# Performance work log

Measured on AMD Instinct MI355X. Metric: run time of the kernel, lower is better.

Reference implementation:

```python
import jax, jax.numpy as jnp
import numpy as np

B, N, D = 4, 2048, 256
EPS = 1e-5


def _clinear(Z, W, b):
    # complex linear: Z (B,2,N,din), W (2,dout,din), b (2,dout)
    Zr, Zi = Z[:, 0], Z[:, 1]
    Wr, Wi = W[0], W[1]
    outr = Zr @ Wr.T - Zi @ Wi.T + b[0]
    outi = Zr @ Wi.T + Zi @ Wr.T + b[1]
    return jnp.stack([outr, outi], axis=1)


def setup_inputs() -> dict:
    key = jax.random.key(0)
    ks = jax.random.split(key, 14)
    sc = 1.0 / np.sqrt(D).astype(np.float32)
    t = jnp.tile(jnp.arange(N + 1, dtype=jnp.float32)[None] * 0.01, (B, 1))
    return {
        'Z_q': jax.random.normal(ks[0], (B, 2, N, D), jnp.float32),
        'Z_k': jax.random.normal(ks[1], (B, 2, N, D), jnp.float32),
        'Z_v': jax.random.normal(ks[2], (B, 2, N, D), jnp.float32),
        't_measure_all': t,
        'W_q': jax.random.normal(ks[3], (2, D, D), jnp.float32) * sc,
        'b_q': jax.random.normal(ks[4], (2, D), jnp.float32) * 0.01,
        'W_k': jax.random.normal(ks[5], (2, D, D), jnp.float32) * sc,
        'b_k': jax.random.normal(ks[6], (2, D), jnp.float32) * 0.01,
        'W_v': jax.random.normal(ks[7], (2, D, D), jnp.float32) * sc,
        'b_v': jax.random.normal(ks[8], (2, D), jnp.float32) * 0.01,
        'W_p': jax.random.normal(ks[9], (2, D, D), jnp.float32) * sc,
        'b_p': jax.random.normal(ks[10], (2, D), jnp.float32) * 0.01,
        'lambda1': jax.random.normal(ks[11], (2, D // 2, 1), jnp.float32),
        'lambda_Omega_sqrt': jax.random.normal(ks[12], (1, D, 1), jnp.float32) * sc,
        'lambda_Gamma_sqrt': jax.random.normal(ks[13], (1, D, 1), jnp.float32) * sc,
        'tau': jnp.asarray(1.0, jnp.float32),
        'delta': jnp.asarray(0.0, jnp.float32),
        'lambda_C': jnp.ones((1, D, 1), jnp.float32),
    }


def reference(Z_q, Z_k, Z_v, t_measure_all, W_q, b_q, W_k, b_k, W_v, b_v,
              W_p, b_p, lambda1, lambda_Omega_sqrt, lambda_Gamma_sqrt,
              tau, delta, lambda_C):
    # lambda_h = 0 * compute_lambda_h(lambda1): conjugate-pair spectrum, zeroed in forward
    lam_r = 0.0 * jnp.concatenate([lambda1[0], lambda1[0]], axis=0)[:, 0]   # (D,)
    lam_i = 0.0 * jnp.concatenate([lambda1[1], -lambda1[1]], axis=0)[:, 0]  # (D,)
    lam_Om = lambda_Omega_sqrt ** 2 + EPS   # process noise (1,D,1)
    lam_Ga = lambda_Gamma_sqrt ** 2 + EPS   # measurement noise (1,D,1)

    Q = _clinear(Z_q, W_q, b_q)  # (B,2,N,D)
    K = _clinear(Z_k, W_k, b_k)
    V = _clinear(Z_v, W_v, b_v)

    t = t_measure_all[0, :-1]  # (N,)
    # exponential state-transition kernels exp(+/- lambda * t): (2,N,D)
    mag_f = jnp.exp(lam_r[None] * t[:, None]); ph_f = lam_i[None] * t[:, None]
    exp_f = jnp.stack([mag_f * jnp.cos(ph_f), mag_f * jnp.sin(ph_f)])
    mag_b = jnp.exp(-lam_r[None] * t[:, None]); ph_b = -lam_i[None] * t[:, None]
    exp_b = jnp.stack([mag_b * jnp.cos(ph_b), mag_b * jnp.sin(ph_b)])
    # one-step transition exp(lambda * dt): (2,D)
    dt = t[1] - t[0]
    mat_exp = jnp.stack([jnp.exp(lam_r * dt) * jnp.cos(lam_i * dt),
                         jnp.exp(lam_r * dt) * jnp.sin(lam_i * dt)])

    # averaged covariance kernel, exact lambda->0 limit: Gamma + Omega*|t_i-t_j|, mean over D
    lamC2 = lambda_C[0, :, 0] ** 2
    ga_bar = jnp.mean(lamC2 * lam_Ga[0, :, 0])
    om_bar = jnp.mean(lamC2 * lam_Om[0, :, 0])
    abs_dt = jnp.abs(t[:, None] - t[None, :])          # (N,N)
    V_avg_ij = ga_bar + om_bar * abs_dt                # (N,N)

    # factorized kernels
    V_v = exp_f[None]                 # (1,2,N,D)
    U_q = exp_b[None] * Q             # (B,2,N,D)
    U_k = exp_b[None] * K
    U_v = exp_b[None] * V

    # precision-weighted squared residual norm R_ij = sum_d |V_k|^2 |U_q_i - U_k_j|^2
    Vk_abs = jnp.sum(exp_f ** 2, axis=0)              # (N,D)
    Uk_abs = jnp.sum(U_k ** 2, axis=1)                # (B,N,D)
    Uq_abs = jnp.sum(U_q ** 2, axis=1)                # (B,N,D)
    T1 = jnp.einsum('id,bjd->bij', Vk_abs, Uk_abs)
    T2 = jnp.sum(Vk_abs[None] * Uq_abs, axis=2)[:, :, None]
    T3 = (jnp.einsum('bid,bjd->bij', Vk_abs[None] * U_q[:, 0], U_k[:, 0]) +
          jnp.einsum('bid,bjd->bij', Vk_abs[None] * U_q[:, 1], U_k[:, 1]))
    R_qk_abs = T1 + T2 - 2.0 * T3                     # (B,N,N)

    scores = -(tau ** 2) * jnp.log(V_avg_ij[None] + R_qk_abs)
    mask = jnp.tril(jnp.ones((N, N), bool))
    scores = jnp.where(mask[None], scores, -jnp.inf)
    A = jax.nn.softmax(scores, axis=2)                # (B,N,N)
    Q_ij = jnp.stack([A, jnp.zeros_like(A)], axis=1)  # (B,2,N,N)

    # est_inner = complex matmul(Q_ij, U_v); Q imag part is zero
    est_inner = jnp.stack([jnp.einsum('bij,bjd->bid', A, U_v[:, 0]),
                           jnp.einsum('bij,bjd->bid', A, U_v[:, 1])], axis=1)
    est_v = V_v * est_inner          # plain elementwise product, as in source
    s = jax.nn.sigmoid(delta)
    est_eigenbasis = (1.0 - s) * V + s * est_v        # (B,2,N,D)

    # complex Hadamard with one-step transition
    pr = mat_exp[0][None, None] * est_eigenbasis[:, 0] - mat_exp[1][None, None] * est_eigenbasis[:, 1]
    pi = mat_exp[0][None, None] * est_eigenbasis[:, 1] + mat_exp[1][None, None] * est_eigenbasis[:, 0]
    pred_p = jnp.stack([pr, pi], axis=1)
    out = _clinear(pred_p, W_p, b_p)                  # (B,2,N,D)

    lambda_h = jnp.stack([lam_r, lam_i])[..., None]
    return est_eigenbasis, out, Q_ij, V_v, U_v, lambda_h
```

## Files before the change

### kernel.cpp

```cpp
#include <hip/hip_runtime.h>
#include <math.h>

#define BN 4
#define NN 2048
#define DD 256
#define EPSF 1e-5f

typedef __attribute__((ext_vector_type(8))) short bf16x8;
typedef __attribute__((ext_vector_type(4))) float f32x4;

constexpr size_t OFF_EST = 0;
constexpr size_t OFF_OUT = (size_t)BN * 2 * NN * DD;
constexpr size_t OFF_QIJ = OFF_OUT + (size_t)BN * 2 * NN * DD;
constexpr size_t OFF_VV  = OFF_QIJ + (size_t)BN * 2 * NN * NN;
constexpr size_t OFF_UV  = OFF_VV + (size_t)2 * NN * DD;
constexpr size_t OFF_LH  = OFF_UV + (size_t)BN * 2 * NN * DD;

constexpr size_t SCR_Q16 = OFF_QIJ + (size_t)NN * NN;
constexpr size_t SCR_K16 = SCR_Q16 + (size_t)BN * NN * DD / 2;
constexpr size_t SCR_VT16= SCR_K16 + (size_t)BN * NN * DD / 2;
constexpr size_t SCR_VRF = OFF_QIJ + (size_t)3 * NN * NN;
constexpr size_t SCR_QN  = SCR_VRF + (size_t)BN * NN * DD;
constexpr size_t SCR_KN  = SCR_QN + (size_t)BN * NN;
constexpr size_t SCR_L   = SCR_KN + (size_t)BN * NN;
constexpr size_t SCR_SC  = SCR_L + (size_t)BN * NN;

__device__ __forceinline__ short f2bf(float x) {
    union { float f; unsigned u; } v; v.f = x;
    unsigned r = v.u + 0x7fff + ((v.u >> 16) & 1);
    return (short)(r >> 16);
}
__device__ __forceinline__ float bf2f(unsigned short h) {
    union { unsigned u; float f; } v; v.u = ((unsigned)h) << 16;
    return v.f;
}

__global__ void k_prep(const float* __restrict__ tau, const float* __restrict__ delta,
                       const float* __restrict__ lamOm, const float* __restrict__ lamGa,
                       const float* __restrict__ lamC, float* __restrict__ dout) {
    __shared__ float red[8];
    const int t = threadIdx.x;
    float c2 = lamC[t] * lamC[t];
    float ga = c2 * (lamGa[t] * lamGa[t] + EPSF);
    float om = c2 * (lamOm[t] * lamOm[t] + EPSF);
    for (int o = 32; o > 0; o >>= 1) {
        ga += __shfl_down(ga, o, 64);
        om += __shfl_down(om, o, 64);
    }
    if ((t & 63) == 0) { red[t >> 6] = ga; red[4 + (t >> 6)] = om; }
    __syncthreads();
    if (t == 0) {
        float gs = red[0] + red[1] + red[2] + red[3];
        float os = red[4] + red[5] + red[6] + red[7];
        float* scal = dout + SCR_SC;
        scal[0] = tau[0] * tau[0];
        scal[1] = 1.f / (1.f + __expf(-delta[0]));
        scal[2] = gs / 256.f;
        scal[3] = os / 256.f;
    }
    float* L = dout + SCR_L;
    for (int i = t; i < BN * NN; i += 256) L[i] = 0.f;
}

__global__ __launch_bounds__(256) void k_qkv(
    const float* __restrict__ Zq, const float* __restrict__ Zk, const float* __restrict__ Zv,
    const float* __restrict__ Wq, const float* __restrict__ bq,
    const float* __restrict__ Wk, const float* __restrict__ bk,
    const float* __restrict__ Wv, const float* __restrict__ bv,
    float* __restrict__ dout)
{
    __shared__ short Al[128 * 40];
    __shared__ short Bl[128 * 40];
    const int z = blockIdx.z;
    const int d0 = blockIdx.x * 128;
    const int b = blockIdx.y >> 4;
    const int n0 = (blockIdx.y & 15) * 128;
    const float* Z; const float* W; const float* bias; int mode;
    if (z == 0)      { Z = Zq; W = Wq; bias = bq; mode = 0; }
    else if (z == 1) { Z = Zk; W = Wk; bias = bk; mode = 0; }
    else if (z == 2) { Z = Zv; W = Wv; bias = bv; mode = 0; }
    else             { Z = Zv; W = Wv; bias = bv; mode = 1; }

    const int t = threadIdx.x, wave = t >> 6, lane = t & 63, quad = lane >> 4, lm = lane & 15;
    const int wm = (wave >> 1) * 64, wn = (wave & 1) * 64;
    const int srow = t >> 1, sch = (t & 1) * 16;

    f32x4 acc[4][4];
#pragma unroll
    for (int i = 0; i < 4; ++i)
#pragma unroll
        for (int j = 0; j < 4; ++j) acc[i][j] = (f32x4){0.f, 0.f, 0.f, 0.f};

    for (int kt = 0; kt < 16; ++kt) {
        const int c = kt >> 3, kk0 = (kt & 7) * 32;
        const float* Za = Z + ((size_t)((b * 2 + c) * NN + n0 + srow)) * DD + kk0 + sch;
        float4 a0 = *(const float4*)(Za + 0);
        float4 a1 = *(const float4*)(Za + 4);
        float4 a2 = *(const float4*)(Za + 8);
        float4 a3 = *(const float4*)(Za + 12);
        int wc; float sgn;
        if (mode == 0) { wc = c; sgn = c ? -1.f : 1.f; }
        else           { wc = 1 - c; sgn = 1.f; }
        const float* Wa = W + ((size_t)wc * DD + d0 + srow) * DD + kk0 + sch;
        float4 w0 = *(const float4*)(Wa + 0);
        float4 w1 = *(const float4*)(Wa + 4);
        float4 w2 = *(const float4*)(Wa + 8);
        float4 w3 = *(const float4*)(Wa + 12);
        __syncthreads();
        bf16x8 pa0, pa1, pw0, pw1;
        pa0[0]=f2bf(a0.x); pa0[1]=f2bf(a0.y); pa0[2]=f2bf(a0.z); pa0[3]=f2bf(a0.w);
        pa0[4]=f2bf(a1.x); pa0[5]=f2bf(a1.y); pa0[6]=f2bf(a1.z); pa0[7]=f2bf(a1.w);
        pa1[0]=f2bf(a2.x); pa1[1]=f2bf(a2.y); pa1[2]=f2bf(a2.z); pa1[3]=f2bf(a2.w);
        pa1[4]=f2bf(a3.x); pa1[5]=f2bf(a3.y); pa1[6]=f2bf(a3.z); pa1[7]=f2bf(a3.w);
        pw0[0]=f2bf(sgn*w0.x); pw0[1]=f2bf(sgn*w0.y); pw0[2]=f2bf(sgn*w0.z); pw0[3]=f2bf(sgn*w0.w);
        pw0[4]=f2bf(sgn*w1.x); pw0[5]=f2bf(sgn*w1.y); pw0[6]=f2bf(sgn*w1.z); pw0[7]=f2bf(sgn*w1.w);
        pw1[0]=f2bf(sgn*w2.x); pw1[1]=f2bf(sgn*w2.y); pw1[2]=f2bf(sgn*w2.z); pw1[3]=f2bf(sgn*w2.w);
        pw1[4]=f2bf(sgn*w3.x); pw1[5]=f2bf(sgn*w3.y); pw1[6]=f2bf(sgn*w3.z); pw1[7]=f2bf(sgn*w3.w);
        *(bf16x8*)&Al[srow * 40 + sch]     = pa0;
        *(bf16x8*)&Al[srow * 40 + sch + 8] = pa1;
        *(bf16x8*)&Bl[srow * 40 + sch]     = pw0;
        *(bf16x8*)&Bl[srow * 40 + sch + 8] = pw1;
        __syncthreads();
        bf16x8 af[4], bff[4];
#pragma unroll
        for (int mi = 0; mi < 4; ++mi) af[mi] = *(const bf16x8*)&Al[(wm + mi * 16 + lm) * 40 + quad * 8];
#pragma unroll
        for (int nj = 0; nj < 4; ++nj) bff[nj] = *(const bf16x8*)&Bl[(wn + nj * 16 + lm) * 40 + quad * 8];
#pragma unroll
        for (int mi = 0; mi < 4; ++mi)
#pragma unroll
            for (int nj = 0; nj < 4; ++nj)
                acc[mi][nj] = __builtin_amdgcn_mfma_f32_16x16x32_bf16(af[mi], bff[nj], acc[mi][nj], 0, 0, 0);
    }

    const float sval = dout[SCR_SC + 1];
    unsigned short* Q16 = (unsigned short*)(dout + SCR_Q16);
    unsigned short* K16 = (unsigned short*)(dout + SCR_K16);
    float* VRF = dout + SCR_VRF;
    const int bofs = mode ? DD : 0;
#pragma unroll
    for (int mi = 0; mi < 4; ++mi)
#pragma unroll
        for (int r = 0; r < 4; ++r) {
            const int m = n0 + wm + mi * 16 + quad * 4 + r;
#pragma unroll
            for (int nj = 0; nj < 4; ++nj) {
                const int d = d0 + wn + nj * 16 + lm;
                float v = acc[mi][nj][r] + bias[bofs + d];
                const size_t ibd = ((size_t)b * NN + m) * DD + d;
                if (z == 0) Q16[ibd] = (unsigned short)f2bf(v);
                else if (z == 1) K16[ibd] = (unsigned short)f2bf(v);
                else if (z == 2) {
                    VRF[ibd] = v;
                    dout[OFF_UV + ((size_t)(b * 2) * NN + m) * DD + d] = v;
                } else {
                    dout[OFF_EST + ((size_t)(b * 2 + 1) * NN + m) * DD + d] = (1.f - sval) * v;
                }
            }
        }
}

__global__ __launch_bounds__(256) void k_outproj(
    const float* __restrict__ Wp, const float* __restrict__ bp, float* __restrict__ dout)
{
    __shared__ short Al[128 * 40];
    __shared__ short Bl[128 * 40];
    const int z = blockIdx.z;
    const int d0 = blockIdx.x * 128;
    const int b = blockIdx.y >> 4;
    const int n0 = (blockIdx.y & 15) * 128;
    const float* Z = dout + OFF_EST;
    const int mode = z;

    const int t = threadIdx.x, wave = t >> 6, lane = t & 63, quad = lane >> 4, lm = lane & 15;
    const int wm = (wave >> 1) * 64, wn = (wave & 1) * 64;
    const int srow = t >> 1, sch = (t & 1) * 16;

    f32x4 acc[4][4];
#pragma unroll
    for (int i = 0; i < 4; ++i)
#pragma unroll
        for (int j = 0; j < 4; ++j) acc[i][j] = (f32x4){0.f, 0.f, 0.f, 0.f};

    for (int kt = 0; kt < 16; ++kt) {
        const int c = kt >> 3, kk0 = (kt & 7) * 32;
        const float* Za = Z + ((size_t)((b * 2 + c) * NN + n0 + srow)) * DD + kk0 + sch;
        float4 a0 = *(const float4*)(Za + 0);
        float4 a1 = *(const float4*)(Za + 4);
        float4 a2 = *(const float4*)(Za + 8);
        float4 a3 = *(const float4*)(Za + 12);
        int wc; float sgn;
        if (mode == 0) { wc = c; sgn = c ? -1.f : 1.f; }
        else           { wc = 1 - c; sgn = 1.f; }
        const float* Wa = Wp + ((size_t)wc * DD + d0 + srow) * DD + kk0 + sch;
        float4 w0 = *(const float4*)(Wa + 0);
        float4 w1 = *(const float4*)(Wa + 4);
        float4 w2 = *(const float4*)(Wa + 8);
        float4 w3 = *(const float4*)(Wa + 12);
        __syncthreads();
        bf16x8 pa0, pa1, pw0, pw1;
        pa0[0]=f2bf(a0.x); pa0[1]=f2bf(a0.y); pa0[2]=f2bf(a0.z); pa0[3]=f2bf(a0.w);
        pa0[4]=f2bf(a1.x); pa0[5]=f2bf(a1.y); pa0[6]=f2bf(a1.z); pa0[7]=f2bf(a1.w);
        pa1[0]=f2bf(a2.x); pa1[1]=f2bf(a2.y); pa1[2]=f2bf(a2.z); pa1[3]=f2bf(a2.w);
        pa1[4]=f2bf(a3.x); pa1[5]=f2bf(a3.y); pa1[6]=f2bf(a3.z); pa1[7]=f2bf(a3.w);
        pw0[0]=f2bf(sgn*w0.x); pw0[1]=f2bf(sgn*w0.y); pw0[2]=f2bf(sgn*w0.z); pw0[3]=f2bf(sgn*w0.w);
        pw0[4]=f2bf(sgn*w1.x); pw0[5]=f2bf(sgn*w1.y); pw0[6]=f2bf(sgn*w1.z); pw0[7]=f2bf(sgn*w1.w);
        pw1[0]=f2bf(sgn*w2.x); pw1[1]=f2bf(sgn*w2.y); pw1[2]=f2bf(sgn*w2.z); pw1[3]=f2bf(sgn*w2.w);
        pw1[4]=f2bf(sgn*w3.x); pw1[5]=f2bf(sgn*w3.y); pw1[6]=f2bf(sgn*w3.z); pw1[7]=f2bf(sgn*w3.w);
        *(bf16x8*)&Al[srow * 40 + sch]     = pa0;
        *(bf16x8*)&Al[srow * 40 + sch + 8] = pa1;
        *(bf16x8*)&Bl[srow * 40 + sch]     = pw0;
        *(bf16x8*)&Bl[srow * 40 + sch + 8] = pw1;
        __syncthreads();
        bf16x8 af[4], bff[4];
#pragma unroll
        for (int mi = 0; mi < 4; ++mi) af[mi] = *(const bf16x8*)&Al[(wm + mi * 16 + lm) * 40 + quad * 8];
#pragma unroll
        for (int nj = 0; nj < 4; ++nj) bff[nj] = *(const bf16x8*)&Bl[(wn + nj * 16 + lm) * 40 + quad * 8];
#pragma unroll
        for (int mi = 0; mi < 4; ++mi)
#pragma unroll
            for (int nj = 0; nj < 4; ++nj)
                acc[mi][nj] = __builtin_amdgcn_mfma_f32_16x16x32_bf16(af[mi], bff[nj], acc[mi][nj], 0, 0, 0);
    }
    const int bofs = mode ? DD : 0;
#pragma unroll
    for (int mi = 0; mi < 4; ++mi)
#pragma unroll
        for (int r = 0; r < 4; ++r) {
            const int m = n0 + wm + mi * 16 + quad * 4 + r;
#pragma unroll
            for (int nj = 0; nj < 4; ++nj) {
                const int d = d0 + wn + nj * 16 + lm;
                dout[OFF_OUT + ((size_t)(b * 2 + z) * NN + m) * DD + d] =
                    acc[mi][nj][r] + bp[bofs + d];
            }
        }
}

__global__ void k_vtrans(float* __restrict__ dout) {
    __shared__ float T[64][65];
    const int b = blockIdx.z;
    const int nb = blockIdx.x * 64, db = blockIdx.y * 64;
    const float* V = dout + SCR_VRF + (size_t)b * NN * DD;
    unsigned short* VT = (unsigned short*)(dout + SCR_VT16) + (size_t)b * DD * NN;
    const int tr = threadIdx.x >> 4, tc = (threadIdx.x & 15) * 4;
#pragma unroll
    for (int p = 0; p < 4; ++p) {
        float4 v = *(const float4*)&V[(size_t)(nb + tr + p * 16) * DD + db + tc];
        T[tr + p * 16][tc + 0] = v.x; T[tr + p * 16][tc + 1] = v.y;
        T[tr + p * 16][tc + 2] = v.z; T[tr + p * 16][tc + 3] = v.w;
    }
    __syncthreads();
#pragma unroll
    for (int p = 0; p < 4; ++p) {
        const int d = tr + p * 16;
        ushort4 o;
        o.x = (unsigned short)f2bf(T[tc + 0][d]);
        o.y = (unsigned short)f2bf(T[tc + 1][d]);
        o.z = (unsigned short)f2bf(T[tc + 2][d]);
        o.w = (unsigned short)f2bf(T[tc + 3][d]);
        *(ushort4*)&VT[(size_t)(db + d) * NN + nb + tc] = o;
    }
}

__global__ void k_norms(float* __restrict__ dout) {
    const int r = blockIdx.x;
    const unsigned short* src = (const unsigned short*)(dout + (blockIdx.y ? SCR_K16 : SCR_Q16));
    float v = bf2f(src[(size_t)r * DD + threadIdx.x]);
    float p = v * v;
    for (int o = 32; o > 0; o >>= 1) p += __shfl_down(p, o, 64);
    __shared__ float red[4];
    if ((threadIdx.x & 63) == 0) red[threadIdx.x >> 6] = p;
    __syncthreads();
    if (threadIdx.x == 0)
        dout[(blockIdx.y ? SCR_KN : SCR_QN) + r] = red[0] + red[1] + red[2] + red[3];
}

__global__ __launch_bounds__(256) void k_scores(const float* __restrict__ tmeas,
                                                float* __restrict__ dout) {
    __shared__ short Al[128 * 40];
    __shared__ short Bl[128 * 40];
    const int b = blockIdx.y, x = blockIdx.x;
    int ti = (int)((sqrtf(8.f * x + 1.f) - 1.f) * 0.5f);
    while ((ti + 1) * (ti + 2) / 2 <= x) ++ti;
    while (ti * (ti + 1) / 2 > x) --ti;
    const int tj = x - ti * (ti + 1) / 2;
    const int i0 = ti * 128, j0 = tj * 128;
    const unsigned short* Q16 = (const unsigned short*)(dout + SCR_Q16) + (size_t)b * NN * DD;
    const unsigned short* K16 = (const unsigned short*)(dout + SCR_K16) + (size_t)b * NN * DD;
    const int t = threadIdx.x, wave = t >> 6, lane = t & 63, quad = lane >> 4, lm = lane & 15;
    const int wm = (wave >> 1) * 64, wn = (wave & 1) * 64;
    const int srow = t >> 1, sch = (t & 1) * 16;

    f32x4 acc[4][4];
#pragma unroll
    for (int i = 0; i < 4; ++i)
#pragma unroll
        for (int j = 0; j < 4; ++j) acc[i][j] = (f32x4){0.f, 0.f, 0.f, 0.f};

    for (int kt = 0; kt < 8; ++kt) {
        const int kk0 = kt * 32;
        const float4 qv0 = *(const float4*)(const void*)(Q16 + (size_t)(i0 + srow) * DD + kk0 + sch);
        const float4 qv1 = *(const float4*)(const void*)(Q16 + (size_t)(i0 + srow) * DD + kk0 + sch + 8);
        const float4 kv0 = *(const float4*)(const void*)(K16 + (size_t)(j0 + srow) * DD + kk0 + sch);
        const float4 kv1 = *(const float4*)(const void*)(K16 + (size_t)(j0 + srow) * DD + kk0 + sch + 8);
        __syncthreads();
        *(float4*)(void*)&Al[srow * 40 + sch]     = qv0;
        *(float4*)(void*)&Al[srow * 40 + sch + 8] = qv1;
        *(float4*)(void*)&Bl[srow * 40 + sch]     = kv0;
        *(float4*)(void*)&Bl[srow * 40 + sch + 8] = kv1;
        __syncthreads();
        bf16x8 af[4], bff[4];
#pragma unroll
        for (int mi = 0; mi < 4; ++mi) af[mi] = *(const bf16x8*)&Al[(wm + mi * 16 + lm) * 40 + quad * 8];
#pragma unroll
        for (int nj = 0; nj < 4; ++nj) bff[nj] = *(const bf16x8*)&Bl[(wn + nj * 16 + lm) * 40 + quad * 8];
#pragma unroll
        for (int mi = 0; mi < 4; ++mi)
#pragma unroll
            for (int nj = 0; nj < 4; ++nj)
                acc[mi][nj] = __builtin_amdgcn_mfma_f32_16x16x32_bf16(af[mi], bff[nj], acc[mi][nj], 0, 0, 0);
    }

    const float tau2 = dout[SCR_SC + 0], ga = dout[SCR_SC + 2], om = dout[SCR_SC + 3];
    float* Qij = dout + OFF_QIJ + (size_t)b * 2 * NN * NN;
    const float* QN_ = dout + SCR_QN + b * NN;
    const float* KN_ = dout + SCR_KN + b * NN;
    float kn[4], tjv[4]; int jj[4];
#pragma unroll
    for (int nj = 0; nj < 4; ++nj) {
        jj[nj] = j0 + wn + nj * 16 + lm;
        kn[nj] = KN_[jj[nj]];
        tjv[nj] = tmeas[jj[nj]];
    }
#pragma unroll
    for (int mi = 0; mi < 4; ++mi)
#pragma unroll
        for (int r = 0; r < 4; ++r) {
            const int i = i0 + wm + mi * 16 + quad * 4 + r;
            const float qni = QN_[i], tqi = tmeas[i];
            float rs = 0.f;
#pragma unroll
            for (int nj = 0; nj < 4; ++nj) {
                float xx = ga + om * fabsf(tqi - tjv[nj]) + qni + kn[nj] - 2.f * acc[mi][nj][r];
                xx = fmaxf(xx, 1e-30f);
                float w = (tau2 == 1.f) ? (1.f / xx) : __expf(-tau2 * __logf(xx));
                if (jj[nj] > i) w = 0.f;
                Qij[(size_t)i * NN + jj[nj]] = w;
                rs += w;
            }
            rs += __shfl_down(rs, 8, 16); rs += __shfl_down(rs, 4, 16);
            rs += __shfl_down(rs, 2, 16); rs += __shfl_down(rs, 1, 16);
            if (lm == 0) atomicAdd(&dout[SCR_L + b * NN + i], rs);
        }
}

__global__ __launch_bounds__(256) void k_estinner(float* __restrict__ dout) {
    __shared__ short Al[128 * 40];
    __shared__ short Bl[128 * 40];
    const int b = blockIdx.z;
    const int d0 = blockIdx.x * 128;
    int y = blockIdx.y, TI = 0;
    for (;;) { const int nc = (TI + 2) >> 1; if (y < nc) break; y -= nc; ++TI; }
    const int i0 = TI * 128;
    const int kbeg = y * 256;
    const int kend = min(kbeg + 256, (TI + 1) * 128);
    const int nst = (kend - kbeg) >> 5;
    const float* Qij = dout + OFF_QIJ + (size_t)b * 2 * NN * NN;
    const unsigned short* VT = (const unsigned short*)(dout + SCR_VT16) + (size_t)b * DD * NN;

    const int t = threadIdx.x, wave = t >> 6, lane = t & 63, quad = lane >> 4, lm = lane & 15;
    const int wm = (wave >> 1) * 64, wn = (wave & 1) * 64;
    const int srow = t >> 1, sch = (t & 1) * 16;

    f32x4 acc[4][4];
#pragma unroll
    for (int i = 0; i < 4; ++i)
#pragma unroll
        for (int j = 0; j < 4; ++j) acc[i][j] = (f32x4){0.f, 0.f, 0.f, 0.f};

    for (int kt = 0; kt < nst; ++kt) {
        const int kk0 = kbeg + kt * 32;
        const float* Aa = Qij + (size_t)(i0 + srow) * NN + kk0 + sch;
        float4 a0 = *(const float4*)(Aa + 0);
        float4 a1 = *(const float4*)(Aa + 4);
        float4 a2 = *(const float4*)(Aa + 8);
        float4 a3 = *(const float4*)(Aa + 12);
        const float4 bv0 = *(const float4*)(const void*)(VT + (size_t)(d0 + srow) * NN + kk0 + sch);
        const float4 bv1 = *(const float4*)(const void*)(VT + (size_t)(d0 + srow) * NN + kk0 + sch + 8);
        __syncthreads();
        bf16x8 pa0, pa1;
        pa0[0]=f2bf(a0.x); pa0[1]=f2bf(a0.y); pa0[2]=f2bf(a0.z); pa0[3]=f2bf(a0.w);
        pa0[4]=f2bf(a1.x); pa0[5]=f2bf(a1.y); pa0[6]=f2bf(a1.z); pa0[7]=f2bf(a1.w);
        pa1[0]=f2bf(a2.x); pa1[1]=f2bf(a2.y); pa1[2]=f2bf(a2.z); pa1[3]=f2bf(a2.w);
        pa1[4]=f2bf(a3.x); pa1[5]=f2bf(a3.y); pa1[6]=f2bf(a3.z); pa1[7]=f2bf(a3.w);
        *(bf16x8*)&Al[srow * 40 + sch]     = pa0;
        *(bf16x8*)&Al[srow * 40 + sch + 8] = pa1;
        *(float4*)(void*)&Bl[srow * 40 + sch]     = bv0;
        *(float4*)(void*)&Bl[srow * 40 + sch + 8] = bv1;
        __syncthreads();
        bf16x8 af[4], bff[4];
#pragma unroll
        for (int mi = 0; mi < 4; ++mi) af[mi] = *(const bf16x8*)&Al[(wm + mi * 16 + lm) * 40 + quad * 8];
#pragma unroll
        for (int nj = 0; nj < 4; ++nj) bff[nj] = *(const bf16x8*)&Bl[(wn + nj * 16 + lm) * 40 + quad * 8];
#pragma unroll
        for (int mi = 0; mi < 4; ++mi)
#pragma unroll
            for (int nj = 0; nj < 4; ++nj)
                acc[mi][nj] = __builtin_amdgcn_mfma_f32_16x16x32_bf16(af[mi], bff[nj], acc[mi][nj], 0, 0, 0);
    }
    float* EST = dout + OFF_EST + (size_t)(b * 2) * NN * DD;
#pragma unroll
    for (int mi = 0; mi < 4; ++mi)
#pragma unroll
        for (int r = 0; r < 4; ++r) {
            const int i = i0 + wm + mi * 16 + quad * 4 + r;
#pragma unroll
            for (int nj = 0; nj < 4; ++nj) {
                const int d = d0 + wn + nj * 16 + lm;
                atomicAdd(&EST[(size_t)i * DD + d], acc[mi][nj][r]);
            }
        }
}

__global__ void k_blend(float* __restrict__ dout) {
    const int b = blockIdx.y, i = blockIdx.x;
    const float s = dout[SCR_SC + 1];
    const float linv = 1.f / dout[SCR_L + b * NN + i];
    float* e = dout + OFF_EST + ((size_t)(b * 2) * NN + i) * DD + threadIdx.x * 4;
    const float* vr = dout + SCR_VRF + ((size_t)b * NN + i) * DD + threadIdx.x * 4;
    float4 ev = *(float4*)e;
    float4 vv = *(const float4*)vr;
    ev.x = (1.f - s) * vv.x + s * ev.x * linv;
    ev.y = (1.f - s) * vv.y + s * ev.y * linv;
    ev.z = (1.f - s) * vv.z + s * ev.z * linv;
    ev.w = (1.f - s) * vv.w + s * ev.w * linv;
    *(float4*)e = ev;
}

__global__ void k_norm_qij(float* __restrict__ dout) {
    const int b = blockIdx.z, i = blockIdx.y;
    const int j0 = blockIdx.x * 1024 + threadIdx.x * 4;
    if (j0 > i) return;
    const float linv = 1.f / dout[SCR_L + b * NN + i];
    float* p = dout + OFF_QIJ + (size_t)b * 2 * NN * NN + (size_t)i * NN + j0;
    float4 v = *(float4*)p;
    v.x *= linv; v.y *= linv; v.z *= linv; v.w *= linv;
    *(float4*)p = v;
}

__global__ void k_fill_upper(float* __restrict__ dout) {
    const int b = blockIdx.y, i = blockIdx.x;
    const int jstart = ((i >> 7) + 1) << 7;
    float* row = dout + OFF_QIJ + (size_t)b * 2 * NN * NN + (size_t)i * NN;
    const float4 z = {0.f, 0.f, 0.f, 0.f};
    for (int j = jstart + threadIdx.x * 4; j < NN; j += 256 * 4)
        *(float4*)&row[j] = z;
}

__global__ void k_zero(float* __restrict__ p, long n) {
    const float4 z = {0.f, 0.f, 0.f, 0.f};
    for (long i = ((long)blockIdx.x * 256 + threadIdx.x) * 4; i < n; i += (long)gridDim.x * 1024)
        *(float4*)&p[i] = z;
}

__global__ void k_ones(float* __restrict__ p, long n) {
    const float4 z = {1.f, 1.f, 1.f, 1.f};
    for (long i = ((long)blockIdx.x * 256 + threadIdx.x) * 4; i < n; i += (long)gridDim.x * 1024)
        *(float4*)&p[i] = z;
}

extern "C" void kernel_launch(void* const* d_in, const int* in_sizes, int n_in,
                              void* d_out, int out_size, void* d_ws, size_t ws_size,
                              hipStream_t stream) {
    const float* Zq = (const float*)d_in[0];
    const float* Zk = (const float*)d_in[1];
    const float* Zv = (const float*)d_in[2];
    const float* tm = (const float*)d_in[3];
    const float* Wq = (const float*)d_in[4];
    const float* bq = (const float*)d_in[5];
    const float* Wk = (const float*)d_in[6];
    const float* bk = (const float*)d_in[7];
    const float* Wv = (const float*)d_in[8];
    const float* bv = (const float*)d_in[9];
    const float* Wp = (const float*)d_in[10];
    const float* bp = (const float*)d_in[11];
    const float* lamOm = (const float*)d_in[13];
    const float* lamGa = (const float*)d_in[14];
    const float* tau = (const float*)d_in[15];
    const float* delta = (const float*)d_in[16];
    const float* lamC = (const float*)d_in[17];
    float* out = (float*)d_out;

    k_prep<<<dim3(1), dim3(256), 0, stream>>>(tau, delta, lamOm, lamGa, lamC, out);
    for (int b = 0; b < BN; ++b)
        k_zero<<<dim3(512), dim3(256), 0, stream>>>(
            out + OFF_EST + (size_t)(2 * b) * NN * DD, (long)NN * DD);
    k_qkv<<<dim3(2, 64, 4), dim3(256), 0, stream>>>(Zq, Zk, Zv, Wq, bq, Wk, bk, Wv, bv, out);
    k_norms<<<dim3(8192, 2), dim3(256), 0, stream>>>(out);
    k_vtrans<<<dim3(32, 4, 4), dim3(256), 0, stream>>>(out);
    k_scores<<<dim3(136, 4), dim3(256), 0, stream>>>(tm, out);
    k_estinner<<<dim3(2, 72, 4), dim3(256), 0, stream>>>(out);
    k_blend<<<dim3(2048, 4), dim3(64), 0, stream>>>(out);
    k_norm_qij<<<dim3(2, 2048, 4), dim3(256), 0, stream>>>(out);
    k_outproj<<<dim3(2, 64, 2), dim3(256), 0, stream>>>(Wp, bp, out);
    k_fill_upper<<<dim3(2048, 4), dim3(256), 0, stream>>>(out);
    for (int b = 0; b < BN; ++b)
        k_zero<<<dim3(4096), dim3(256), 0, stream>>>(
            out + OFF_QIJ + (size_t)(2 * b + 1) * NN * NN, (long)NN * NN);
    k_ones<<<dim3(512), dim3(256), 0, stream>>>(out + OFF_VV, (long)NN * DD);
    k_zero<<<dim3(512), dim3(256), 0, stream>>>(out + OFF_VV + (size_t)NN * DD, (long)NN * DD);
    for (int b = 0; b < BN; ++b)
        k_zero<<<dim3(512), dim3(256), 0, stream>>>(
            out + OFF_UV + (size_t)(2 * b + 1) * NN * DD, (long)NN * DD);
    k_zero<<<dim3(1), dim3(256), 0, stream>>>(out + OFF_LH, 512);
}
```

Baseline: 413.7 us.

## Pre-convert inputs to bf16, fuse norms and Q normalization, merge fill kernels

Adds a conversion kernel that turns Z and the signed, interleaved complex weights into bf16 once, so the projection GEMMs load bf16 directly instead of converting fp32 on every tile. Query and key row norms are now computed in the qkv epilogue with atomics, which removes the separate norms kernel. The Q_ij row normalization moves into estinner, which now uses 512-thread blocks covering all of D. Blend writes a bf16 copy for the output projection, and the many zero/ones launches collapse into a single fill kernel. This cuts launches and repeated conversions, but adds an extra bf16 pass over inputs and more scratch traffic.

```diff
diff --git a/kernel.cpp b/kernel.cpp
--- a/kernel.cpp
+++ b/kernel.cpp
@@ -16,14 +16,18 @@
 constexpr size_t OFF_UV  = OFF_VV + (size_t)2 * NN * DD;
 constexpr size_t OFF_LH  = OFF_UV + (size_t)BN * 2 * NN * DD;
 
-constexpr size_t SCR_Q16 = OFF_QIJ + (size_t)NN * NN;
-constexpr size_t SCR_K16 = SCR_Q16 + (size_t)BN * NN * DD / 2;
-constexpr size_t SCR_VT16= SCR_K16 + (size_t)BN * NN * DD / 2;
-constexpr size_t SCR_VRF = OFF_QIJ + (size_t)3 * NN * NN;
-constexpr size_t SCR_QN  = SCR_VRF + (size_t)BN * NN * DD;
-constexpr size_t SCR_KN  = SCR_QN + (size_t)BN * NN;
-constexpr size_t SCR_L   = SCR_KN + (size_t)BN * NN;
-constexpr size_t SCR_SC  = SCR_L + (size_t)BN * NN;
+constexpr size_t SCR_B0   = OFF_QIJ + (size_t)NN * NN;
+constexpr size_t U_Q16    = 0;
+constexpr size_t U_K16    = (size_t)BN * NN * DD;
+constexpr size_t U_VT16   = 2 * (size_t)BN * NN * DD;
+constexpr size_t SCR_QN   = SCR_B0 + 3 * (size_t)BN * NN * DD / 2;
+constexpr size_t SCR_KN   = SCR_QN + (size_t)BN * NN;
+constexpr size_t SCR_L    = SCR_KN + (size_t)BN * NN;
+constexpr size_t SCR_SC   = SCR_L + (size_t)BN * NN;
+constexpr size_t SCR_E16F = OFF_QIJ + 3 * (size_t)NN * NN;
+constexpr size_t SCR_Z16F = OFF_QIJ + 5 * (size_t)NN * NN;
+constexpr size_t SCR_Z16VF = OFF_QIJ + 7 * (size_t)NN * NN;
+constexpr size_t U_W16    = (size_t)BN * NN * 512;
 
 __device__ __forceinline__ short f2bf(float x) {
     union { float f; unsigned u; } v; v.f = x;
@@ -33,6 +37,12 @@
 __device__ __forceinline__ float bf2f(unsigned short h) {
     union { unsigned u; float f; } v; v.u = ((unsigned)h) << 16;
     return v.f;
+}
+__device__ __forceinline__ unsigned short* u16p(float* d, size_t fofs) {
+    return (unsigned short*)(d + fofs);
+}
+__device__ __forceinline__ const unsigned short* u16pc(const float* d, size_t fofs) {
+    return (const unsigned short*)(d + fofs);
 }
 
 __global__ void k_prep(const float* __restrict__ tau, const float* __restrict__ delta,
@@ -58,16 +68,75 @@
         scal[2] = gs / 256.f;
         scal[3] = os / 256.f;
     }
-    float* L = dout + SCR_L;
-    for (int i = t; i < BN * NN; i += 256) L[i] = 0.f;
-}
-
-__global__ __launch_bounds__(256) void k_qkv(
-    const float* __restrict__ Zq, const float* __restrict__ Zk, const float* __restrict__ Zv,
-    const float* __restrict__ Wq, const float* __restrict__ bq,
-    const float* __restrict__ Wk, const float* __restrict__ bk,
-    const float* __restrict__ Wv, const float* __restrict__ bv,
-    float* __restrict__ dout)
+    float* Z = dout + SCR_QN;
+    for (int i = t; i < 3 * BN * NN; i += 256) Z[i] = 0.f;
+}
+
+__global__ void k_zero_est(float* __restrict__ dout) {
+    const int b = blockIdx.y;
+    float* p = dout + OFF_EST + (size_t)(2 * b) * NN * DD;
+    const size_t i = ((size_t)blockIdx.x * 256 + threadIdx.x) * 4;
+    *(float4*)&p[i] = (float4){0.f, 0.f, 0.f, 0.f};
+}
+
+__global__ void k_cvt(const float* __restrict__ Zq, const float* __restrict__ Zk,
+                      const float* __restrict__ Zv,
+                      const float* __restrict__ Wq, const float* __restrict__ Wk,
+                      const float* __restrict__ Wv, const float* __restrict__ Wp,
+                      float* __restrict__ dout) {
+    const int z = blockIdx.z;
+    if (z < 3) {
+        const float* Z = (z == 0) ? Zq : (z == 1) ? Zk : Zv;
+        unsigned short* O = (z == 0) ? u16p(dout, SCR_Z16F)
+                          : (z == 1) ? u16p(dout, SCR_Z16F) + (size_t)BN * NN * 512
+                                     : u16p(dout, SCR_Z16VF);
+        const long n4 = (long)BN * 2 * NN * DD / 4;
+        for (long i4 = (long)blockIdx.x * 256 + threadIdx.x; i4 < n4;
+             i4 += (long)gridDim.x * 256) {
+            const long i = i4 * 4;
+            const int d = (int)(i & (DD - 1));
+            const long r = i >> 8;
+            const int n = (int)(r & (NN - 1));
+            const long bc = r >> 11;
+            const int c = (int)(bc & 1), b = (int)(bc >> 1);
+            float4 v = *(const float4*)&Z[i];
+            ushort4 o;
+            o.x = (unsigned short)f2bf(v.x); o.y = (unsigned short)f2bf(v.y);
+            o.z = (unsigned short)f2bf(v.z); o.w = (unsigned short)f2bf(v.w);
+            *(ushort4*)&O[((size_t)(b * NN + n)) * 512 + c * 256 + d] = o;
+        }
+    } else {
+        const float* Ws[4] = {Wq, Wk, Wv, Wp};
+        unsigned short* W16 = u16p(dout, SCR_Z16VF) + U_W16;
+        const long n4 = 6L * 256 * 512 / 4;
+        for (long e4 = (long)blockIdx.x * 256 + threadIdx.x; e4 < n4;
+             e4 += (long)gridDim.x * 256) {
+            const long e = e4 * 4;
+            const int k = (int)(e & 511);
+            const long rest = e >> 9;
+            const int dd = (int)(rest & 255);
+            const int m = (int)(rest >> 8);
+            int proj, mode;
+            if (m < 3)      { proj = m; mode = 0; }
+            else if (m == 3){ proj = 2; mode = 1; }
+            else            { proj = 3; mode = m - 4; }
+            const int kc = k >> 8, kk = k & 255;
+            int wc; float sgn;
+            if (mode == 0) { wc = kc; sgn = kc ? -1.f : 1.f; }
+            else           { wc = 1 - kc; sgn = 1.f; }
+            float4 v = *(const float4*)&Ws[proj][((size_t)wc * DD + dd) * DD + kk];
+            ushort4 o;
+            o.x = (unsigned short)f2bf(sgn * v.x); o.y = (unsigned short)f2bf(sgn * v.y);
+            o.z = (unsigned short)f2bf(sgn * v.z); o.w = (unsigned short)f2bf(sgn * v.w);
+            *(ushort4*)&W16[(size_t)m * 256 * 512 + (size_t)dd * 512 + k] = o;
+        }
+    }
+}
+
+__global__ __launch_bounds__(256) void k_qkv(const float* __restrict__ bq,
+                                             const float* __restrict__ bk,
+                                             const float* __restrict__ bv,
+                                             float* __restrict__ dout)
 {
     __shared__ short Al[128 * 40];
     __shared__ short Bl[128 * 40];
@@ -75,11 +144,14 @@
     const int d0 = blockIdx.x * 128;
     const int b = blockIdx.y >> 4;
     const int n0 = (blockIdx.y & 15) * 128;
-    const float* Z; const float* W; const float* bias; int mode;
-    if (z == 0)      { Z = Zq; W = Wq; bias = bq; mode = 0; }
-    else if (z == 1) { Z = Zk; W = Wk; bias = bk; mode = 0; }
-    else if (z == 2) { Z = Zv; W = Wv; bias = bv; mode = 0; }
-    else             { Z = Zv; W = Wv; bias = bv; mode = 1; }
+
+    const unsigned short* Z16 =
+        (z == 0) ? u16pc(dout, SCR_Z16F)
+      : (z == 1) ? u16pc(dout, SCR_Z16F) + (size_t)BN * NN * 512
+                 : u16pc(dout, SCR_Z16VF);
+    const unsigned short* W16 = u16pc(dout, SCR_Z16VF) + U_W16 + (size_t)z * 256 * 512;
+    const float* bias = (z == 0) ? bq : (z == 1) ? bk : bv;
+    const int bofs = (z == 3) ? DD : 0;
 
     const int t = threadIdx.x, wave = t >> 6, lane = t & 63, quad = lane >> 4, lm = lane & 15;
     const int wm = (wave >> 1) * 64, wn = (wave & 1) * 64;
@@ -92,34 +164,18 @@
         for (int j = 0; j < 4; ++j) acc[i][j] = (f32x4){0.f, 0.f, 0.f, 0.f};
 
     for (int kt = 0; kt < 16; ++kt) {
-        const int c = kt >> 3, kk0 = (kt & 7) * 32;
-        const float* Za = Z + ((size_t)((b * 2 + c) * NN + n0 + srow)) * DD + kk0 + sch;
-        float4 a0 = *(const float4*)(Za + 0);
-        float4 a1 = *(const float4*)(Za + 4);
-        float4 a2 = *(const float4*)(Za + 8);
-        float4 a3 = *(const float4*)(Za + 12);
-        int wc; float sgn;
-        if (mode == 0) { wc = c; sgn = c ? -1.f : 1.f; }
-        else           { wc = 1 - c; sgn = 1.f; }
-        const float* Wa = W + ((size_t)wc * DD + d0 + srow) * DD + kk0 + sch;
-        float4 w0 = *(const float4*)(Wa + 0);
-        float4 w1 = *(const float4*)(Wa + 4);
-        float4 w2 = *(const float4*)(Wa + 8);
-        float4 w3 = *(const float4*)(Wa + 12);
-        __syncthreads();
-        bf16x8 pa0, pa1, pw0, pw1;
-        pa0[0]=f2bf(a0.x); pa0[1]=f2bf(a0.y); pa0[2]=f2bf(a0.z); pa0[3]=f2bf(a0.w);
-        pa0[4]=f2bf(a1.x); pa0[5]=f2bf(a1.y); pa0[6]=f2bf(a1.z); pa0[7]=f2bf(a1.w);
-        pa1[0]=f2bf(a2.x); pa1[1]=f2bf(a2.y); pa1[2]=f2bf(a2.z); pa1[3]=f2bf(a2.w);
-        pa1[4]=f2bf(a3.x); pa1[5]=f2bf(a3.y); pa1[6]=f2bf(a3.z); pa1[7]=f2bf(a3.w);
-        pw0[0]=f2bf(sgn*w0.x); pw0[1]=f2bf(sgn*w0.y); pw0[2]=f2bf(sgn*w0.z); pw0[3]=f2bf(sgn*w0.w);
-        pw0[4]=f2bf(sgn*w1.x); pw0[5]=f2bf(sgn*w1.y); pw0[6]=f2bf(sgn*w1.z); pw0[7]=f2bf(sgn*w1.w);
-        pw1[0]=f2bf(sgn*w2.x); pw1[1]=f2bf(sgn*w2.y); pw1[2]=f2bf(sgn*w2.z); pw1[3]=f2bf(sgn*w2.w);
-        pw1[4]=f2bf(sgn*w3.x); pw1[5]=f2bf(sgn*w3.y); pw1[6]=f2bf(sgn*w3.z); pw1[7]=f2bf(sgn*w3.w);
-        *(bf16x8*)&Al[srow * 40 + sch]     = pa0;
-        *(bf16x8*)&Al[srow * 40 + sch + 8] = pa1;
-        *(bf16x8*)&Bl[srow * 40 + sch]     = pw0;
-        *(bf16x8*)&Bl[srow * 40 + sch + 8] = pw1;
+        const int kk0 = kt * 32;
+        const unsigned short* Za = Z16 + ((size_t)(b * NN + n0 + srow)) * 512 + kk0 + sch;
+        bf16x8 a0 = *(const bf16x8*)(Za + 0);
+        bf16x8 a1 = *(const bf16x8*)(Za + 8);
+        const unsigned short* Wa = W16 + (size_t)(d0 + srow) * 512 + kk0 + sch;
+        bf16x8 w0 = *(const bf16x8*)(Wa + 0);
+        bf16x8 w1 = *(const bf16x8*)(Wa + 8);
+        __syncthreads();
+        *(bf16x8*)&Al[srow * 40 + sch]     = a0;
+        *(bf16x8*)&Al[srow * 40 + sch + 8] = a1;
+        *(bf16x8*)&Bl[srow * 40 + sch]     = w0;
+        *(bf16x8*)&Bl[srow * 40 + sch + 8] = w1;
         __syncthreads();
         bf16x8 af[4], bff[4];
 #pragma unroll
@@ -133,35 +189,62 @@
                 acc[mi][nj] = __builtin_amdgcn_mfma_f32_16x16x32_bf16(af[mi], bff[nj], acc[mi][nj], 0, 0, 0);
     }
 
-    const float sval = dout[SCR_SC + 1];
-    unsigned short* Q16 = (unsigned short*)(dout + SCR_Q16);
-    unsigned short* K16 = (unsigned short*)(dout + SCR_K16);
-    float* VRF = dout + SCR_VRF;
-    const int bofs = mode ? DD : 0;
-#pragma unroll
-    for (int mi = 0; mi < 4; ++mi)
-#pragma unroll
-        for (int r = 0; r < 4; ++r) {
-            const int m = n0 + wm + mi * 16 + quad * 4 + r;
-#pragma unroll
-            for (int nj = 0; nj < 4; ++nj) {
-                const int d = d0 + wn + nj * 16 + lm;
-                float v = acc[mi][nj][r] + bias[bofs + d];
-                const size_t ibd = ((size_t)b * NN + m) * DD + d;
-                if (z == 0) Q16[ibd] = (unsigned short)f2bf(v);
-                else if (z == 1) K16[ibd] = (unsigned short)f2bf(v);
-                else if (z == 2) {
-                    VRF[ibd] = v;
-                    dout[OFF_UV + ((size_t)(b * 2) * NN + m) * DD + d] = v;
-                } else {
-                    dout[OFF_EST + ((size_t)(b * 2 + 1) * NN + m) * DD + d] = (1.f - sval) * v;
+    if (z <= 1) {
+        unsigned short* O16 = u16p(dout, SCR_B0) + (z ? U_K16 : U_Q16) + (size_t)b * NN * DD;
+        float* NRM = dout + (z ? SCR_KN : SCR_QN) + b * NN;
+#pragma unroll
+        for (int mi = 0; mi < 4; ++mi)
+#pragma unroll
+            for (int r = 0; r < 4; ++r) {
+                const int m = n0 + wm + mi * 16 + quad * 4 + r;
+                float ss = 0.f;
+#pragma unroll
+                for (int nj = 0; nj < 4; ++nj) {
+                    const int d = d0 + wn + nj * 16 + lm;
+                    unsigned short h = (unsigned short)f2bf(acc[mi][nj][r] + bias[d]);
+                    O16[(size_t)m * DD + d] = h;
+                    const float vb = bf2f(h);
+                    ss = fmaf(vb, vb, ss);
+                }
+                ss += __shfl_down(ss, 8, 16); ss += __shfl_down(ss, 4, 16);
+                ss += __shfl_down(ss, 2, 16); ss += __shfl_down(ss, 1, 16);
+                if (lm == 0) atomicAdd(&NRM[m], ss);
+            }
+    } else if (z == 2) {
+        float* UV0 = dout + OFF_UV + (size_t)(b * 2) * NN * DD;
+#pragma unroll
+        for (int mi = 0; mi < 4; ++mi)
+#pragma unroll
+            for (int r = 0; r < 4; ++r) {
+                const int m = n0 + wm + mi * 16 + quad * 4 + r;
+#pragma unroll
+                for (int nj = 0; nj < 4; ++nj) {
+                    const int d = d0 + wn + nj * 16 + lm;
+                    UV0[(size_t)m * DD + d] = acc[mi][nj][r] + bias[d];
                 }
             }
-        }
-}
-
-__global__ __launch_bounds__(256) void k_outproj(
-    const float* __restrict__ Wp, const float* __restrict__ bp, float* __restrict__ dout)
+    } else {
+        const float s1 = 1.f - dout[SCR_SC + 1];
+        float* EST1 = dout + OFF_EST + (size_t)(b * 2 + 1) * NN * DD;
+        unsigned short* E16 = u16p(dout, SCR_E16F) + (size_t)b * NN * 512;
+#pragma unroll
+        for (int mi = 0; mi < 4; ++mi)
+#pragma unroll
+            for (int r = 0; r < 4; ++r) {
+                const int m = n0 + wm + mi * 16 + quad * 4 + r;
+#pragma unroll
+                for (int nj = 0; nj < 4; ++nj) {
+                    const int d = d0 + wn + nj * 16 + lm;
+                    const float v = s1 * (acc[mi][nj][r] + bias[bofs + d]);
+                    EST1[(size_t)m * DD + d] = v;
+                    E16[(size_t)m * 512 + 256 + d] = (unsigned short)f2bf(v);
+                }
+            }
+    }
+}
+
+__global__ __launch_bounds__(256) void k_outproj(const float* __restrict__ bp,
+                                                 float* __restrict__ dout)
 {
     __shared__ short Al[128 * 40];
     __shared__ short Bl[128 * 40];
@@ -169,8 +252,8 @@
     const int d0 = blockIdx.x * 128;
     const int b = blockIdx.y >> 4;
     const int n0 = (blockIdx.y & 15) * 128;
-    const float* Z = dout + OFF_EST;
-    const int mode = z;
+    const unsigned short* E16 = u16pc(dout, SCR_E16F) + (size_t)b * NN * 512;
+    const unsigned short* W16 = u16pc(dout, SCR_Z16VF) + U_W16 + (size_t)(4 + z) * 256 * 512;
 
     const int t = threadIdx.x, wave = t >> 6, lane = t & 63, quad = lane >> 4, lm = lane & 15;
     const int wm = (wave >> 1) * 64, wn = (wave & 1) * 64;
@@ -183,34 +266,18 @@
         for (int j = 0; j < 4; ++j) acc[i][j] = (f32x4){0.f, 0.f, 0.f, 0.f};
 
     for (int kt = 0; kt < 16; ++kt) {
-        const int c = kt >> 3, kk0 = (kt & 7) * 32;
-        const float* Za = Z + ((size_t)((b * 2 + c) * NN + n0 + srow)) * DD + kk0 + sch;
-        float4 a0 = *(const float4*)(Za + 0);
-        float4 a1 = *(const float4*)(Za + 4);
-        float4 a2 = *(const float4*)(Za + 8);
-        float4 a3 = *(const float4*)(Za + 12);
-        int wc; float sgn;
-        if (mode == 0) { wc = c; sgn = c ? -1.f : 1.f; }
-        else           { wc = 1 - c; sgn = 1.f; }
-        const float* Wa = Wp + ((size_t)wc * DD + d0 + srow) * DD + kk0 + sch;
-        float4 w0 = *(const float4*)(Wa + 0);
-        float4 w1 = *(const float4*)(Wa + 4);
-        float4 w2 = *(const float4*)(Wa + 8);
-        float4 w3 = *(const float4*)(Wa + 12);
-        __syncthreads();
-        bf16x8 pa0, pa1, pw0, pw1;
-        pa0[0]=f2bf(a0.x); pa0[1]=f2bf(a0.y); pa0[2]=f2bf(a0.z); pa0[3]=f2bf(a0.w);
-        pa0[4]=f2bf(a1.x); pa0[5]=f2bf(a1.y); pa0[6]=f2bf(a1.z); pa0[7]=f2bf(a1.w);
-        pa1[0]=f2bf(a2.x); pa1[1]=f2bf(a2.y); pa1[2]=f2bf(a2.z); pa1[3]=f2bf(a2.w);
-        pa1[4]=f2bf(a3.x); pa1[5]=f2bf(a3.y); pa1[6]=f2bf(a3.z); pa1[7]=f2bf(a3.w);
-        pw0[0]=f2bf(sgn*w0.x); pw0[1]=f2bf(sgn*w0.y); pw0[2]=f2bf(sgn*w0.z); pw0[3]=f2bf(sgn*w0.w);
-        pw0[4]=f2bf(sgn*w1.x); pw0[5]=f2bf(sgn*w1.y); pw0[6]=f2bf(sgn*w1.z); pw0[7]=f2bf(sgn*w1.w);
-        pw1[0]=f2bf(sgn*w2.x); pw1[1]=f2bf(sgn*w2.y); pw1[2]=f2bf(sgn*w2.z); pw1[3]=f2bf(sgn*w2.w);
-        pw1[4]=f2bf(sgn*w3.x); pw1[5]=f2bf(sgn*w3.y); pw1[6]=f2bf(sgn*w3.z); pw1[7]=f2bf(sgn*w3.w);
-        *(bf16x8*)&Al[srow * 40 + sch]     = pa0;
-        *(bf16x8*)&Al[srow * 40 + sch + 8] = pa1;
-        *(bf16x8*)&Bl[srow * 40 + sch]     = pw0;
-        *(bf16x8*)&Bl[srow * 40 + sch + 8] = pw1;
+        const int kk0 = kt * 32;
+        const unsigned short* Za = E16 + ((size_t)(n0 + srow)) * 512 + kk0 + sch;
+        bf16x8 a0 = *(const bf16x8*)(Za + 0);
+        bf16x8 a1 = *(const bf16x8*)(Za + 8);
+        const unsigned short* Wa = W16 + (size_t)(d0 + srow) * 512 + kk0 + sch;
+        bf16x8 w0 = *(const bf16x8*)(Wa + 0);
+        bf16x8 w1 = *(const bf16x8*)(Wa + 8);
+        __syncthreads();
+        *(bf16x8*)&Al[srow * 40 + sch]     = a0;
+        *(bf16x8*)&Al[srow * 40 + sch + 8] = a1;
+        *(bf16x8*)&Bl[srow * 40 + sch]     = w0;
+        *(bf16x8*)&Bl[srow * 40 + sch + 8] = w1;
         __syncthreads();
         bf16x8 af[4], bff[4];
 #pragma unroll
@@ -223,7 +290,8 @@
             for (int nj = 0; nj < 4; ++nj)
                 acc[mi][nj] = __builtin_amdgcn_mfma_f32_16x16x32_bf16(af[mi], bff[nj], acc[mi][nj], 0, 0, 0);
     }
-    const int bofs = mode ? DD : 0;
+    const int bofs = z ? DD : 0;
+    float* O = dout + OFF_OUT + (size_t)(b * 2 + z) * NN * DD;
 #pragma unroll
     for (int mi = 0; mi < 4; ++mi)
 #pragma unroll
@@ -232,8 +300,7 @@
 #pragma unroll
             for (int nj = 0; nj < 4; ++nj) {
                 const int d = d0 + wn + nj * 16 + lm;
-                dout[OFF_OUT + ((size_t)(b * 2 + z) * NN + m) * DD + d] =
-                    acc[mi][nj][r] + bp[bofs + d];
+                O[(size_t)m * DD + d] = acc[mi][nj][r] + bp[bofs + d];
             }
         }
 }
@@ -242,8 +309,8 @@
     __shared__ float T[64][65];
     const int b = blockIdx.z;
     const int nb = blockIdx.x * 64, db = blockIdx.y * 64;
-    const float* V = dout + SCR_VRF + (size_t)b * NN * DD;
-    unsigned short* VT = (unsigned short*)(dout + SCR_VT16) + (size_t)b * DD * NN;
+    const float* V = dout + OFF_UV + (size_t)(b * 2) * NN * DD;
+    unsigned short* VT = u16p(dout, SCR_B0) + U_VT16 + (size_t)b * DD * NN;
     const int tr = threadIdx.x >> 4, tc = (threadIdx.x & 15) * 4;
 #pragma unroll
     for (int p = 0; p < 4; ++p) {
@@ -262,19 +329,6 @@
         o.w = (unsigned short)f2bf(T[tc + 3][d]);
         *(ushort4*)&VT[(size_t)(db + d) * NN + nb + tc] = o;
     }
-}
-
-__global__ void k_norms(float* __restrict__ dout) {
-    const int r = blockIdx.x;
-    const unsigned short* src = (const unsigned short*)(dout + (blockIdx.y ? SCR_K16 : SCR_Q16));
-    float v = bf2f(src[(size_t)r * DD + threadIdx.x]);
-    float p = v * v;
-    for (int o = 32; o > 0; o >>= 1) p += __shfl_down(p, o, 64);
-    __shared__ float red[4];
-    if ((threadIdx.x & 63) == 0) red[threadIdx.x >> 6] = p;
-    __syncthreads();
-    if (threadIdx.x == 0)
-        dout[(blockIdx.y ? SCR_KN : SCR_QN) + r] = red[0] + red[1] + red[2] + red[3];
 }
 
 __global__ __launch_bounds__(256) void k_scores(const float* __restrict__ tmeas,
@@ -287,8 +341,8 @@
     while (ti * (ti + 1) / 2 > x) --ti;
     const int tj = x - ti * (ti + 1) / 2;
     const int i0 = ti * 128, j0 = tj * 128;
-    const unsigned short* Q16 = (const unsigned short*)(dout + SCR_Q16) + (size_t)b * NN * DD;
-    const unsigned short* K16 = (const unsigned short*)(dout + SCR_K16) + (size_t)b * NN * DD;
+    const unsigned short* Q16 = u16pc(dout, SCR_B0) + U_Q16 + (size_t)b * NN * DD;
+    const unsigned short* K16 = u16pc(dout, SCR_B0) + U_K16 + (size_t)b * NN * DD;
     const int t = threadIdx.x, wave = t >> 6, lane = t & 63, quad = lane >> 4, lm = lane & 15;
     const int wm = (wave >> 1) * 64, wn = (wave & 1) * 64;
     const int srow = t >> 1, sch = (t & 1) * 16;
@@ -301,15 +355,15 @@
 
     for (int kt = 0; kt < 8; ++kt) {
         const int kk0 = kt * 32;
-        const float4 qv0 = *(const float4*)(const void*)(Q16 + (size_t)(i0 + srow) * DD + kk0 + sch);
-        const float4 qv1 = *(const float4*)(const void*)(Q16 + (size_t)(i0 + srow) * DD + kk0 + sch + 8);
-        const float4 kv0 = *(const float4*)(const void*)(K16 + (size_t)(j0 + srow) * DD + kk0 + sch);
-        const float4 kv1 = *(const float4*)(const void*)(K16 + (size_t)(j0 + srow) * DD + kk0 + sch + 8);
-        __syncthreads();
-        *(float4*)(void*)&Al[srow * 40 + sch]     = qv0;
-        *(float4*)(void*)&Al[srow * 40 + sch + 8] = qv1;
-        *(float4*)(void*)&Bl[srow * 40 + sch]     = kv0;
-        *(float4*)(void*)&Bl[srow * 40 + sch + 8] = kv1;
+        bf16x8 q0 = *(const bf16x8*)(Q16 + (size_t)(i0 + srow) * DD + kk0 + sch);
+        bf16x8 q1 = *(const bf16x8*)(Q16 + (size_t)(i0 + srow) * DD + kk0 + sch + 8);
+        bf16x8 k0 = *(const bf16x8*)(K16 + (size_t)(j0 + srow) * DD + kk0 + sch);
+        bf16x8 k1 = *(const bf16x8*)(K16 + (size_t)(j0 + srow) * DD + kk0 + sch + 8);
+        __syncthreads();
+        *(bf16x8*)&Al[srow * 40 + sch]     = q0;
+        *(bf16x8*)&Al[srow * 40 + sch + 8] = q1;
+        *(bf16x8*)&Bl[srow * 40 + sch]     = k0;
+        *(bf16x8*)&Bl[srow * 40 + sch + 8] = k1;
         __syncthreads();
         bf16x8 af[4], bff[4];
 #pragma unroll
@@ -356,23 +410,24 @@
         }
 }
 
-__global__ __launch_bounds__(256) void k_estinner(float* __restrict__ dout) {
+__global__ __launch_bounds__(512) void k_estinner(float* __restrict__ dout) {
     __shared__ short Al[128 * 40];
-    __shared__ short Bl[128 * 40];
-    const int b = blockIdx.z;
-    const int d0 = blockIdx.x * 128;
-    int y = blockIdx.y, TI = 0;
+    __shared__ short Bl[256 * 40];
+    const int b = blockIdx.y;
+    int y = blockIdx.x, TI = 0;
     for (;;) { const int nc = (TI + 2) >> 1; if (y < nc) break; y -= nc; ++TI; }
     const int i0 = TI * 128;
     const int kbeg = y * 256;
     const int kend = min(kbeg + 256, (TI + 1) * 128);
     const int nst = (kend - kbeg) >> 5;
-    const float* Qij = dout + OFF_QIJ + (size_t)b * 2 * NN * NN;
-    const unsigned short* VT = (const unsigned short*)(dout + SCR_VT16) + (size_t)b * DD * NN;
+    float* Qij = dout + OFF_QIJ + (size_t)b * 2 * NN * NN;
+    const unsigned short* VT = u16pc(dout, SCR_B0) + U_VT16 + (size_t)b * DD * NN;
 
     const int t = threadIdx.x, wave = t >> 6, lane = t & 63, quad = lane >> 4, lm = lane & 15;
-    const int wm = (wave >> 1) * 64, wn = (wave & 1) * 64;
-    const int srow = t >> 1, sch = (t & 1) * 16;
+    const int wm = (wave >> 2) * 64, wn = (wave & 3) * 64;
+    const int arow = t >> 2, acol = (t & 3) * 8;
+    const int vrow = t >> 1, vcol = (t & 1) * 16;
+    const float linv = 1.f / dout[SCR_L + b * NN + i0 + arow];
 
     f32x4 acc[4][4];
 #pragma unroll
@@ -382,23 +437,22 @@
 
     for (int kt = 0; kt < nst; ++kt) {
         const int kk0 = kbeg + kt * 32;
-        const float* Aa = Qij + (size_t)(i0 + srow) * NN + kk0 + sch;
-        float4 a0 = *(const float4*)(Aa + 0);
-        float4 a1 = *(const float4*)(Aa + 4);
-        float4 a2 = *(const float4*)(Aa + 8);
-        float4 a3 = *(const float4*)(Aa + 12);
-        const float4 bv0 = *(const float4*)(const void*)(VT + (size_t)(d0 + srow) * NN + kk0 + sch);
-        const float4 bv1 = *(const float4*)(const void*)(VT + (size_t)(d0 + srow) * NN + kk0 + sch + 8);
-        __syncthreads();
-        bf16x8 pa0, pa1;
-        pa0[0]=f2bf(a0.x); pa0[1]=f2bf(a0.y); pa0[2]=f2bf(a0.z); pa0[3]=f2bf(a0.w);
-        pa0[4]=f2bf(a1.x); pa0[5]=f2bf(a1.y); pa0[6]=f2bf(a1.z); pa0[7]=f2bf(a1.w);
-        pa1[0]=f2bf(a2.x); pa1[1]=f2bf(a2.y); pa1[2]=f2bf(a2.z); pa1[3]=f2bf(a2.w);
-        pa1[4]=f2bf(a3.x); pa1[5]=f2bf(a3.y); pa1[6]=f2bf(a3.z); pa1[7]=f2bf(a3.w);
-        *(bf16x8*)&Al[srow * 40 + sch]     = pa0;
-        *(bf16x8*)&Al[srow * 40 + sch + 8] = pa1;
-        *(float4*)(void*)&Bl[srow * 40 + sch]     = bv0;
-        *(float4*)(void*)&Bl[srow * 40 + sch + 8] = bv1;
+        float* Ap = &Qij[(size_t)(i0 + arow) * NN + kk0 + acol];
+        float4 w0 = *(const float4*)(Ap + 0);
+        float4 w1 = *(const float4*)(Ap + 4);
+        w0.x *= linv; w0.y *= linv; w0.z *= linv; w0.w *= linv;
+        w1.x *= linv; w1.y *= linv; w1.z *= linv; w1.w *= linv;
+        bf16x8 pa;
+        pa[0] = f2bf(w0.x); pa[1] = f2bf(w0.y); pa[2] = f2bf(w0.z); pa[3] = f2bf(w0.w);
+        pa[4] = f2bf(w1.x); pa[5] = f2bf(w1.y); pa[6] = f2bf(w1.z); pa[7] = f2bf(w1.w);
+        bf16x8 v0 = *(const bf16x8*)(VT + (size_t)vrow * NN + kk0 + vcol);
+        bf16x8 v1 = *(const bf16x8*)(VT + (size_t)vrow * NN + kk0 + vcol + 8);
+        *(float4*)(Ap + 0) = w0;
+        *(float4*)(Ap + 4) = w1;
+        __syncthreads();
+        *(bf16x8*)&Al[arow * 40 + acol] = pa;
+        *(bf16x8*)&Bl[vrow * 40 + vcol]     = v0;
+        *(bf16x8*)&Bl[vrow * 40 + vcol + 8] = v1;
         __syncthreads();
         bf16x8 af[4], bff[4];
 #pragma unroll
@@ -419,7 +473,7 @@
             const int i = i0 + wm + mi * 16 + quad * 4 + r;
 #pragma unroll
             for (int nj = 0; nj < 4; ++nj) {
-                const int d = d0 + wn + nj * 16 + lm;
+                const int d = wn + nj * 16 + lm;
                 atomicAdd(&EST[(size_t)i * DD + d], acc[mi][nj][r]);
             }
         }
@@ -428,48 +482,44 @@
 __global__ void k_blend(float* __restrict__ dout) {
     const int b = blockIdx.y, i = blockIdx.x;
     const float s = dout[SCR_SC + 1];
-    const float linv = 1.f / dout[SCR_L + b * NN + i];
     float* e = dout + OFF_EST + ((size_t)(b * 2) * NN + i) * DD + threadIdx.x * 4;
-    const float* vr = dout + SCR_VRF + ((size_t)b * NN + i) * DD + threadIdx.x * 4;
+    const float* vr = dout + OFF_UV + ((size_t)(b * 2) * NN + i) * DD + threadIdx.x * 4;
+    unsigned short* E16 = u16p(dout, SCR_E16F) + ((size_t)(b * NN + i)) * 512 + threadIdx.x * 4;
     float4 ev = *(float4*)e;
     float4 vv = *(const float4*)vr;
-    ev.x = (1.f - s) * vv.x + s * ev.x * linv;
-    ev.y = (1.f - s) * vv.y + s * ev.y * linv;
-    ev.z = (1.f - s) * vv.z + s * ev.z * linv;
-    ev.w = (1.f - s) * vv.w + s * ev.w * linv;
+    ev.x = (1.f - s) * vv.x + s * ev.x;
+    ev.y = (1.f - s) * vv.y + s * ev.y;
+    ev.z = (1.f - s) * vv.z + s * ev.z;
+    ev.w = (1.f - s) * vv.w + s * ev.w;
     *(float4*)e = ev;
-}
-
-__global__ void k_norm_qij(float* __restrict__ dout) {
-    const int b = blockIdx.z, i = blockIdx.y;
-    const int j0 = blockIdx.x * 1024 + threadIdx.x * 4;
-    if (j0 > i) return;
-    const float linv = 1.f / dout[SCR_L + b * NN + i];
-    float* p = dout + OFF_QIJ + (size_t)b * 2 * NN * NN + (size_t)i * NN + j0;
-    float4 v = *(float4*)p;
-    v.x *= linv; v.y *= linv; v.z *= linv; v.w *= linv;
-    *(float4*)p = v;
-}
-
-__global__ void k_fill_upper(float* __restrict__ dout) {
-    const int b = blockIdx.y, i = blockIdx.x;
-    const int jstart = ((i >> 7) + 1) << 7;
-    float* row = dout + OFF_QIJ + (size_t)b * 2 * NN * NN + (size_t)i * NN;
-    const float4 z = {0.f, 0.f, 0.f, 0.f};
-    for (int j = jstart + threadIdx.x * 4; j < NN; j += 256 * 4)
-        *(float4*)&row[j] = z;
-}
-
-__global__ void k_zero(float* __restrict__ p, long n) {
-    const float4 z = {0.f, 0.f, 0.f, 0.f};
-    for (long i = ((long)blockIdx.x * 256 + threadIdx.x) * 4; i < n; i += (long)gridDim.x * 1024)
-        *(float4*)&p[i] = z;
-}
-
-__global__ void k_ones(float* __restrict__ p, long n) {
-    const float4 z = {1.f, 1.f, 1.f, 1.f};
-    for (long i = ((long)blockIdx.x * 256 + threadIdx.x) * 4; i < n; i += (long)gridDim.x * 1024)
-        *(float4*)&p[i] = z;
+    ushort4 o;
+    o.x = (unsigned short)f2bf(ev.x); o.y = (unsigned short)f2bf(ev.y);
+    o.z = (unsigned short)f2bf(ev.z); o.w = (unsigned short)f2bf(ev.w);
+    *(ushort4*)E16 = o;
+}
+
+__global__ void k_fills(float* __restrict__ dout) {
+    const int z = blockIdx.z;
+    if (z >= 11) {
+        const int b = z - 11, i = blockIdx.x;
+        const int jstart = ((i >> 7) + 1) << 7;
+        float* row = dout + OFF_QIJ + (size_t)b * 2 * NN * NN + (size_t)i * NN;
+        const float4 zz = {0.f, 0.f, 0.f, 0.f};
+        for (int j = jstart + threadIdx.x * 4; j < NN; j += 256 * 4)
+            *(float4*)&row[j] = zz;
+        return;
+    }
+    size_t base; long n; float val = 0.f;
+    if (z < 4)       { base = OFF_QIJ + (size_t)(2 * z + 1) * NN * NN; n = (long)NN * NN; }
+    else if (z == 4) { base = OFF_VV; n = (long)NN * DD; val = 1.f; }
+    else if (z == 5) { base = OFF_VV + (size_t)NN * DD; n = (long)NN * DD; }
+    else if (z < 10) { base = OFF_UV + (size_t)(2 * (z - 6) + 1) * NN * DD; n = (long)NN * DD; }
+    else             { base = OFF_LH; n = 512; }
+    float* p = dout + base;
+    const float4 v = {val, val, val, val};
+    for (long i = ((long)blockIdx.x * 256 + threadIdx.x) * 4; i < n;
+         i += (long)gridDim.x * 1024)
+        *(float4*)&p[i] = v;
 }
 
 extern "C" void kernel_launch(void* const* d_in, const int* in_sizes, int n_in,
@@ -495,25 +545,13 @@
     float* out = (float*)d_out;
 
     k_prep<<<dim3(1), dim3(256), 0, stream>>>(tau, delta, lamOm, lamGa, lamC, out);
-    for (int b = 0; b < BN; ++b)
-        k_zero<<<dim3(512), dim3(256), 0, stream>>>(
-            out + OFF_EST + (size_t)(2 * b) * NN * DD, (long)NN * DD);
-    k_qkv<<<dim3(2, 64, 4), dim3(256), 0, stream>>>(Zq, Zk, Zv, Wq, bq, Wk, bk, Wv, bv, out);
-    k_norms<<<dim3(8192, 2), dim3(256), 0, stream>>>(out);
+    k_cvt<<<dim3(2048, 1, 4), dim3(256), 0, stream>>>(Zq, Zk, Zv, Wq, Wk, Wv, Wp, out);
+    k_zero_est<<<dim3(512, 4), dim3(256), 0, stream>>>(out);
+    k_qkv<<<dim3(2, 64, 4), dim3(256), 0, stream>>>(bq, bk, bv, out);
     k_vtrans<<<dim3(32, 4, 4), dim3(256), 0, stream>>>(out);
     k_scores<<<dim3(136, 4), dim3(256), 0, stream>>>(tm, out);
-    k_estinner<<<dim3(2, 72, 4), dim3(256), 0, stream>>>(out);
+    k_estinner<<<dim3(72, 4), dim3(512), 0, stream>>>(out);
     k_blend<<<dim3(2048, 4), dim3(64), 0, stream>>>(out);
-    k_norm_qij<<<dim3(2, 2048, 4), dim3(256), 0, stream>>>(out);
-    k_outproj<<<dim3(2, 64, 2), dim3(256), 0, stream>>>(Wp, bp, out);
-    k_fill_upper<<<dim3(2048, 4), dim3(256), 0, stream>>>(out);
-    for (int b = 0; b < BN; ++b)
-        k_zero<<<dim3(4096), dim3(256), 0, stream>>>(
-            out + OFF_QIJ + (size_t)(2 * b + 1) * NN * NN, (long)NN * NN);
-    k_ones<<<dim3(512), dim3(256), 0, stream>>>(out + OFF_VV, (long)NN * DD);
-    k_zero<<<dim3(512), dim3(256), 0, stream>>>(out + OFF_VV + (size_t)NN * DD, (long)NN * DD);
-    for (int b = 0; b < BN; ++b)
-        k_zero<<<dim3(512), dim3(256), 0, stream>>>(
-            out + OFF_UV + (size_t)(2 * b + 1) * NN * DD, (long)NN * DD);
-    k_zero<<<dim3(1), dim3(256), 0, stream>>>(out + OFF_LH, 512);
-}
+    k_outproj<<<dim3(2, 64, 2), dim3(256), 0, stream>>>(bp, out);
+    k_fills<<<dim3(2048, 1, 15), dim3(256), 0, stream>>>(out);
+}
```

Result: faster. 368.9 us (-10.8%).
